# Performance work log

Hardware: AMD Instinct MI355X
Metric: run time of the kernel (lower is better)

## Reference

```python
import jax, jax.numpy as jnp
import numpy as np

NUM_HEADS = 16
HEAD_DIM = 64
TEMP = 0.001        # temperature for the mask-deriving softmax
THRESH = 0.019      # sparsity threshold
NEG = -1.0e9        # masked_fill value


def setup_inputs() -> dict:
    key = jax.random.key(0)
    ks = jax.random.split(key, 7)
    B, S, D = 4, 1024, 1024
    scale = 1.0 / np.sqrt(D).astype(np.float32)
    inp = {
        "Q": jax.random.normal(ks[0], (B, S, D), jnp.float32),
        "K": jax.random.normal(ks[1], (B, S, D), jnp.float32),
        "V": jax.random.normal(ks[2], (B, S, D), jnp.float32),
        "Wq": jax.random.normal(ks[3], (D, D), jnp.float32) * scale,
        "bq": jnp.zeros((D,), jnp.float32),
        "Wk": jax.random.normal(ks[4], (D, D), jnp.float32) * scale,
        "bk": jnp.zeros((D,), jnp.float32),
        "Wv": jax.random.normal(ks[5], (D, D), jnp.float32) * scale,
        "bv": jnp.zeros((D,), jnp.float32),
        "Wo": jax.random.normal(ks[6], (D, D), jnp.float32) * scale,
        "bo": jnp.zeros((D,), jnp.float32),
    }
    return inp


def reference(Q, K, V, Wq, bq, Wk, bk, Wv, bv, Wo, bo):
    B, S, D = Q.shape

    def split_heads(x):  # [B,S,D] -> [B,H,S,hd]
        return x.reshape(B, S, NUM_HEADS, HEAD_DIM).transpose(0, 2, 1, 3)

    q = split_heads(Q @ Wq + bq)
    k = split_heads(K @ Wk + bk)
    v = split_heads(V @ Wv + bv)

    scores = jnp.einsum('bhqd,bhkd->bhqk', q, k) / np.float32(np.sqrt(HEAD_DIM))
    # temperature-scaled softmax used only to derive a data-dependent mask
    att_map = jax.nn.softmax(scores / TEMP, axis=-1)
    masked_scores = jnp.where(att_map < THRESH, jnp.float32(NEG), scores)
    attn_weights = jax.nn.softmax(masked_scores, axis=-1)

    attn_out = jnp.einsum('bhqk,bhkd->bhqd', attn_weights, v)
    attn_out = attn_out.transpose(0, 2, 1, 3).reshape(B, S, D)
    return attn_out @ Wo + bo
```

## Files before the change

kernel.cpp:

```cpp
#include <hip/hip_runtime.h>
#include <hip/hip_bf16.h>
#include <math.h>

#define SEQ    1024
#define DMODEL 1024
#define NHEAD  16
#define HDIM   64
#define BATCH  4
#define MROWS  4096

typedef float f32x4 __attribute__((ext_vector_type(4)));
typedef short s16x8 __attribute__((ext_vector_type(8)));
typedef _Float16 f16x8 __attribute__((ext_vector_type(8)));

__device__ __forceinline__ float bf2f(unsigned short u) {
    return __uint_as_float(((unsigned int)u) << 16);
}
__device__ __forceinline__ unsigned short f2bf(float f) {
    __hip_bfloat16 h = __float2bfloat16(f);
    return *reinterpret_cast<unsigned short*>(&h);
}
__device__ __forceinline__ unsigned short f2h(float f) {
    _Float16 h = (_Float16)f;
    return *reinterpret_cast<unsigned short*>(&h);
}
__device__ __forceinline__ float h2f(unsigned short u) {
    _Float16 h = *reinterpret_cast<_Float16*>(&u);
    return (float)h;
}
__device__ __forceinline__ void split2(float x, unsigned short& u0, unsigned short& u1) {
    u0 = f2h(x);
    float f0 = h2f(u0);
    u1 = f2h((x - f0) * 2048.0f);
}

__device__ __forceinline__ void gload16(const void* g, void* l) {
    __builtin_amdgcn_global_load_lds(
        (const __attribute__((address_space(1))) unsigned int*)g,
        (__attribute__((address_space(3))) unsigned int*)l, 16, 0, 0);
}

template<int NS>
__global__ __launch_bounds__(256) void splitx_k(const float* __restrict__ X,
                                                unsigned short* __restrict__ P,
                                                int nvec, size_t plane)
{
    const int i = blockIdx.x * 256 + threadIdx.x;
    if (i >= nvec) return;
    const float* src = X + (size_t)i * 8;
    float4 v0 = *(const float4*)src;
    float4 v1 = *(const float4*)(src + 4);
    float x[8] = {v0.x, v0.y, v0.z, v0.w, v1.x, v1.y, v1.z, v1.w};
    unsigned short p0[8], p1[8];
    #pragma unroll
    for (int e = 0; e < 8; ++e) {
        if (NS == 1) { p0[e] = f2bf(x[e]); }
        else         { split2(x[e], p0[e], p1[e]); }
    }
    *(uint4*)(P + (size_t)i * 8) = *(uint4*)p0;
    if (NS == 2) {
        *(uint4*)(P + plane + (size_t)i * 8) = *(uint4*)p1;
    }
}

template<int NS>
__global__ __launch_bounds__(256) void wsplit_k(const float* __restrict__ W,
                                                unsigned short* __restrict__ Wt,
                                                size_t plane)
{
    __shared__ float tile[64][65];
    const int t  = threadIdx.x;
    const int n0 = blockIdx.x * 64;
    const int k0 = blockIdx.y * 64;
    const int col = t & 63;
    const int rq  = t >> 6;

    #pragma unroll
    for (int p = 0; p < 16; ++p) {
        const int row = p * 4 + rq;
        tile[row][col] = W[(size_t)(k0 + row) * DMODEL + n0 + col];
    }
    __syncthreads();
    #pragma unroll
    for (int p = 0; p < 16; ++p) {
        const int nrow = p * 4 + rq;
        const float v = tile[col][nrow];
        const size_t o = (size_t)(n0 + nrow) * DMODEL + k0 + col;
        if (NS == 1) {
            Wt[o] = f2bf(v);
        } else {
            unsigned short u0, u1;
            split2(v, u0, u1);
            Wt[o] = u0; Wt[plane + o] = u1;
        }
    }
}

template<int NS, bool FOLD, bool SPLITOUT>
__global__ __launch_bounds__(256, (NS == 1 ? 4 : 2))
void gemm_planes(const unsigned short* __restrict__ Ab,
                 const unsigned short* __restrict__ Bb,
                 const float* __restrict__ biasp,
                 float* __restrict__ Cp,
                 unsigned short* __restrict__ Pout,
                 float oscale,
                 int M, int N, int K,
                 size_t planeA, size_t planeB,
                 size_t planeO)
{
    __shared__ unsigned short S[2][NS][192][32];

    const int t = threadIdx.x;
    const int w = t >> 6, l = t & 63, g = l >> 4, j = l & 15;
    const int wm = w >> 1;
    const int wn = w & 1;
    const int m0 = blockIdx.y * 128;
    const int n0 = blockIdx.x * 64;

    f32x4 facc[8];
    #pragma unroll
    for (int f = 0; f < 8; ++f) facc[f] = (f32x4){0.f, 0.f, 0.f, 0.f};
    double dacc[8][4] = {};

    const int stgrow = w * 16 + (l >> 2);
    const int stgcol = ((l & 3) ^ ((l >> 3) & 3)) * 8;
    const unsigned short* gA = Ab + (size_t)(m0 + stgrow) * K + stgcol;
    const unsigned short* gB = Bb + (size_t)(n0 + stgrow) * K + stgcol;

    auto stage = [&](int buf, int k0) {
        #pragma unroll
        for (int p = 0; p < NS; ++p) {
            gload16(gA + (size_t)p * planeA + k0,                  &S[buf][p][w * 16][0]);
            gload16(gA + (size_t)p * planeA + (size_t)64 * K + k0, &S[buf][p][64 + w * 16][0]);
            gload16(gB + (size_t)p * planeB + k0,                  &S[buf][p][128 + w * 16][0]);
        }
    };

    const int gs8 = (g ^ ((j >> 1) & 3)) * 8;

    stage(0, 0);
    const int NT = K / 32;
    for (int kt = 0; kt < NT; ++kt) {
        const int cur = kt & 1;
        if (kt + 1 < NT) {
            stage(cur ^ 1, (kt + 1) * 32);
            if constexpr (NS == 2) asm volatile("s_waitcnt vmcnt(6)" ::: "memory");
            else                   asm volatile("s_waitcnt vmcnt(3)" ::: "memory");
        } else {
            asm volatile("s_waitcnt vmcnt(0)" ::: "memory");
        }
        __builtin_amdgcn_sched_barrier(0);
        __builtin_amdgcn_s_barrier();
        __builtin_amdgcn_sched_barrier(0);

        if constexpr (NS == 1) {
            s16x8 a[4];
            #pragma unroll
            for (int mi = 0; mi < 4; ++mi)
                a[mi] = *(const s16x8*)&S[cur][0][wm * 64 + mi * 16 + j][gs8];
            __builtin_amdgcn_s_setprio(1);
            #pragma unroll
            for (int ni = 0; ni < 2; ++ni) {
                const int nr = 128 + wn * 32 + ni * 16 + j;
                s16x8 b0 = *(const s16x8*)&S[cur][0][nr][gs8];
                #pragma unroll
                for (int mi = 0; mi < 4; ++mi) {
                    const int f = mi * 2 + ni;
                    facc[f] = __builtin_amdgcn_mfma_f32_16x16x32_bf16(a[mi], b0, facc[f], 0, 0, 0);
                }
            }
            __builtin_amdgcn_s_setprio(0);
        } else {
            f16x8 a0[4], a1[4];
            #pragma unroll
            for (int mi = 0; mi < 4; ++mi) {
                a0[mi] = *(const f16x8*)&S[cur][0][wm * 64 + mi * 16 + j][gs8];
                a1[mi] = *(const f16x8*)&S[cur][1][wm * 64 + mi * 16 + j][gs8];
            }
            __builtin_amdgcn_s_setprio(1);
            #pragma unroll
            for (int ni = 0; ni < 2; ++ni) {
                const int nr = 128 + wn * 32 + ni * 16 + j;
                f16x8 b0 = *(const f16x8*)&S[cur][0][nr][gs8];
                f16x8 b1 = *(const f16x8*)&S[cur][1][nr][gs8];
                #pragma unroll
                for (int mi = 0; mi < 4; ++mi) {
                    const int f = mi * 2 + ni;
                    f32x4 z = {0.f, 0.f, 0.f, 0.f};
                    z       = __builtin_amdgcn_mfma_f32_16x16x32_f16(a0[mi], b0, z,       0, 0, 0);
                    facc[f] = __builtin_amdgcn_mfma_f32_16x16x32_f16(a0[mi], b1, facc[f], 0, 0, 0);
                    facc[f] = __builtin_amdgcn_mfma_f32_16x16x32_f16(a1[mi], b0, facc[f], 0, 0, 0);
                    #pragma unroll
                    for (int r = 0; r < 4; ++r) dacc[f][r] += (double)z[r];
                }
            }
            __builtin_amdgcn_s_setprio(0);
        }

        __builtin_amdgcn_sched_barrier(0);
        __builtin_amdgcn_s_barrier();
        __builtin_amdgcn_sched_barrier(0);
    }

    #pragma unroll
    for (int ni = 0; ni < 2; ++ni) {
        const int col = n0 + wn * 32 + ni * 16 + j;
        const float bv = biasp[col];
        #pragma unroll
        for (int mi = 0; mi < 4; ++mi) {
            const int f = mi * 2 + ni;
            #pragma unroll
            for (int r = 0; r < 4; ++r) {
                const int row = m0 + wm * 64 + mi * 16 + 4 * g + r;
                float val;
                if (FOLD) val = (float)(dacc[f][r] + (double)facc[f][r] * (1.0 / 2048.0) + (double)bv);
                else      val = facc[f][r] + bv;
                if (SPLITOUT) {
                    const int bq = row >> 10, s = row & 1023;
                    const int h  = col >> 6,  d = col & 63;
                    const size_t o = (((size_t)(bq * 16 + h)) * SEQ + s) * HDIM + d;
                    unsigned short u0, u1;
                    split2(val * oscale, u0, u1);
                    Pout[o] = u0; Pout[planeO + o] = u1;
                } else {
                    Cp[(size_t)row * N + col] = val;
                }
            }
        }
    }
}

#define CAND 32
#define QROWS 128
__global__ __launch_bounds__(512, 4) void attn_k(const unsigned short* __restrict__ q3,
                                                 const unsigned short* __restrict__ k3,
                                                 const float* __restrict__ vf,
                                                 unsigned short* __restrict__ attnb,
                                                 size_t plane)
{
    __shared__ unsigned short Ks[2][64][72];
    __shared__ int   ckey[QROWS][CAND];
    __shared__ float csc[QROWS][CAND];
    __shared__ int   ccnt[QROWS];
    __shared__ float zinv[QROWS];

    const int t  = threadIdx.x;
    const int w  = t >> 6, l = t & 63, g = l >> 4, j = l & 15;
    const int bh = blockIdx.x >> 3;
    const int qt = blockIdx.x & 7;
    const int b  = bh >> 4, h = bh & 15;

    if (t < QROWS) ccnt[t] = 0;

    f16x8 aq[2][2];
    {
        const size_t qoff = ((size_t)bh * SEQ + qt * QROWS + w * 16 + j) * HDIM + g * 8;
        #pragma unroll
        for (int p = 0; p < 2; ++p)
            #pragma unroll
            for (int half = 0; half < 2; ++half)
                aq[p][half] = *(const f16x8*)(q3 + p * plane + qoff + half * 32);
    }

    const int skey = t >> 3;
    const int soff = (t & 7) * 8;
    const unsigned short* ksrc = k3 + (size_t)bh * (SEQ * HDIM) + (size_t)skey * HDIM + soff;

    float rm[4], rz[4];
    #pragma unroll
    for (int r = 0; r < 4; ++r) { rm[r] = -INFINITY; rz[r] = 0.f; }

    for (int ch = 0; ch < 16; ++ch) {
        __syncthreads();
        #pragma unroll
        for (int p = 0; p < 2; ++p) {
            const unsigned short* s = ksrc + p * plane + ch * 4096;
            *(uint4*)&Ks[p][skey][soff] = *(const uint4*)(s);
        }
        __syncthreads();

        float sc[4][4];
        __builtin_amdgcn_s_setprio(1);
        #pragma unroll
        for (int kb = 0; kb < 4; ++kb) {
            f32x4 accM = {0.f,0.f,0.f,0.f};
            f32x4 accC0 = {0.f,0.f,0.f,0.f}, accC1 = {0.f,0.f,0.f,0.f};
            const int kr = kb * 16 + j;
            #pragma unroll
            for (int half = 0; half < 2; ++half) {
                f16x8 b0 = *(const f16x8*)&Ks[0][kr][half * 32 + g * 8];
                f16x8 b1 = *(const f16x8*)&Ks[1][kr][half * 32 + g * 8];
                accM  = __builtin_amdgcn_mfma_f32_16x16x32_f16(aq[0][half], b0, accM,  0, 0, 0);
                accC0 = __builtin_amdgcn_mfma_f32_16x16x32_f16(aq[0][half], b1, accC0, 0, 0, 0);
                accC1 = __builtin_amdgcn_mfma_f32_16x16x32_f16(aq[1][half], b0, accC1, 0, 0, 0);
            }
            #pragma unroll
            for (int r = 0; r < 4; ++r)
                sc[kb][r] = accM[r] + (accC0[r] + accC1[r]) * (1.0f / 2048.0f);
        }
        __builtin_amdgcn_s_setprio(0);

        #pragma unroll
        for (int r = 0; r < 4; ++r) {
            float nmc = fmaxf(fmaxf(sc[0][r], sc[1][r]), fmaxf(sc[2][r], sc[3][r]));
            #pragma unroll
            for (int off = 1; off < 16; off <<= 1) nmc = fmaxf(nmc, __shfl_xor(nmc, off));
            if (__all(nmc <= rm[r] - 0.03f)) continue;
            const float nm = fmaxf(nmc, rm[r]);
            float add = 0.f;
            #pragma unroll
            for (int kb = 0; kb < 4; ++kb) add += __expf((sc[kb][r] - nm) * 1000.f);
            rz[r] = rz[r] * __expf((rm[r] - nm) * 1000.f) + add;
            rm[r] = nm;
            const float thr = nm - 0.004f;
            #pragma unroll
            for (int kb = 0; kb < 4; ++kb) {
                if (sc[kb][r] >= thr) {
                    const int row = w * 16 + 4 * g + r;
                    const int pos = atomicAdd(&ccnt[row], 1);
                    if (pos < CAND) {
                        ckey[row][pos] = ch * 64 + kb * 16 + j;
                        csc[row][pos]  = sc[kb][r];
                    }
                }
            }
        }
    }
    __syncthreads();

    float Zr[4];
    #pragma unroll
    for (int r = 0; r < 4; ++r) {
        float z = rz[r];
        #pragma unroll
        for (int off = 1; off < 16; off <<= 1) z += __shfl_xor(z, off);
        Zr[r] = z;
    }
    #pragma unroll
    for (int r = 0; r < 4; ++r) {
        if (j == r) {
            const int row = w * 16 + 4 * g + r;
            const double cut = (double)rm[r] + 0.001 * log(0.019 * (double)Zr[r]);
            const int craw = ccnt[row];
            const int c = craw < CAND ? craw : CAND;
            int n = 0; float z2 = 0.f;
            for (int i = 0; i < c; ++i) {
                const float s = csc[row][i];
                if ((double)s >= cut) {
                    const float ev = __expf(s - rm[r]);
                    ckey[row][n] = ckey[row][i];
                    csc[row][n]  = ev;
                    z2 += ev; ++n;
                }
            }
            ccnt[row] = (craw > CAND) ? -1 : n;
            zinv[row] = (n > 0) ? 1.f / z2 : 0.f;
        }
    }
    __syncthreads();

    const float* vbase = vf + (size_t)b * SEQ * DMODEL + h * HDIM + l;
    for (int i = 0; i < 16; ++i) {
        const int row = w * 16 + i;
        const int n = ccnt[row];
        float o = 0.f;
        if (n == 0) {
            for (int kk = 0; kk < SEQ; ++kk) o += vbase[(size_t)kk * DMODEL];
            o *= (1.0f / 1024.0f);
        } else if (n < 0) {
            o = INFINITY;
        } else {
            const float inv = zinv[row];
            int i2 = 0;
            for (; i2 + 4 <= n; i2 += 4) {
                const float c0 = csc[row][i2 + 0], c1 = csc[row][i2 + 1];
                const float c2 = csc[row][i2 + 2], c3 = csc[row][i2 + 3];
                const float v0 = vbase[(size_t)ckey[row][i2 + 0] * DMODEL];
                const float v1 = vbase[(size_t)ckey[row][i2 + 1] * DMODEL];
                const float v2 = vbase[(size_t)ckey[row][i2 + 2] * DMODEL];
                const float v3 = vbase[(size_t)ckey[row][i2 + 3] * DMODEL];
                o += c0 * v0; o += c1 * v1; o += c2 * v2; o += c3 * v3;
            }
            for (; i2 < n; ++i2)
                o += csc[row][i2] * vbase[(size_t)ckey[row][i2] * DMODEL];
            o *= inv;
        }
        attnb[((size_t)b * SEQ + qt * QROWS + row) * DMODEL + h * HDIM + l] = f2bf(o);
    }
}

extern "C" void kernel_launch(void* const* d_in, const int* in_sizes, int n_in,
                              void* d_out, int out_size, void* d_ws, size_t ws_size,
                              hipStream_t stream) {
    const float* Q  = (const float*)d_in[0];
    const float* K  = (const float*)d_in[1];
    const float* V  = (const float*)d_in[2];
    const float* Wq = (const float*)d_in[3];
    const float* bq = (const float*)d_in[4];
    const float* Wk = (const float*)d_in[5];
    const float* bk = (const float*)d_in[6];
    const float* Wv = (const float*)d_in[7];
    const float* bv = (const float*)d_in[8];
    const float* Wo = (const float*)d_in[9];
    const float* bo = (const float*)d_in[10];

    const size_t PLANE  = (size_t)MROWS * DMODEL;
    const size_t WPLANE = (size_t)DMODEL * DMODEL;

    unsigned short* Aspl = (unsigned short*)d_ws;
    unsigned short* Wp   = Aspl + 2 * PLANE;
    unsigned short* q3   = Wp + 2 * WPLANE;
    unsigned short* k3   = q3 + 2 * PLANE;
    float*          vf   = (float*)(k3 + 2 * PLANE);
    unsigned short* attnb = Aspl;

    dim3 blk(256, 1, 1);
    dim3 gg(DMODEL / 64, MROWS / 128, 1);
    dim3 gw(DMODEL / 64, DMODEL / 64, 1);
    const int nvec = (int)(PLANE / 8);
    dim3 gs((nvec + 255) / 256, 1, 1);

    splitx_k<2><<<gs, blk, 0, stream>>>(Q, Aspl, nvec, PLANE);
    wsplit_k<2><<<gw, blk, 0, stream>>>(Wq, Wp, WPLANE);
    gemm_planes<2, true, true><<<gg, blk, 0, stream>>>(Aspl, Wp, bq, nullptr, q3, 0.125f,
                                                       MROWS, DMODEL, DMODEL, PLANE, WPLANE, PLANE);
    splitx_k<2><<<gs, blk, 0, stream>>>(K, Aspl, nvec, PLANE);
    wsplit_k<2><<<gw, blk, 0, stream>>>(Wk, Wp, WPLANE);
    gemm_planes<2, true, true><<<gg, blk, 0, stream>>>(Aspl, Wp, bk, nullptr, k3, 1.0f,
                                                       MROWS, DMODEL, DMODEL, PLANE, WPLANE, PLANE);
    splitx_k<1><<<gs, blk, 0, stream>>>(V, Aspl, nvec, PLANE);
    wsplit_k<1><<<gw, blk, 0, stream>>>(Wv, Wp, WPLANE);
    gemm_planes<1, false, false><<<gg, blk, 0, stream>>>(Aspl, Wp, bv, vf, nullptr, 1.0f,
                                                         MROWS, DMODEL, DMODEL, PLANE, WPLANE, PLANE);
    attn_k<<<dim3(64 * 8, 1, 1), dim3(512, 1, 1), 0, stream>>>(q3, k3, vf, attnb, PLANE);

    wsplit_k<1><<<gw, blk, 0, stream>>>(Wo, Wp, WPLANE);
    gemm_planes<1, false, false><<<gg, blk, 0, stream>>>(attnb, Wp, bo, (float*)d_out, nullptr, 1.0f,
                                                         MROWS, DMODEL, DMODEL, PLANE, WPLANE, PLANE);
}
```

Measured before the change: 316.0 us.

## Batch Q and K projections into dual launches and prefetch K chunks in attention

The Q and K split, weight-transpose and GEMM kernels are merged into single launches that use a grid z/y dimension to pick the operand set. This doubles the grid so the GPU is better filled and cuts launch count. The workspace is re-laid out so separate buffers exist for each operand. The GEMM occupancy hint for the two-plane path rises from 2 to 3 waves per SIMD, and the attention kernel now register-prefetches the next K chunk while computing the current one. The costs are more workspace memory, possible register pressure from the higher occupancy bound, and dropped __restrict__ qualifiers on the GEMM inputs.

```diff
diff --git a/kernel.cpp b/kernel.cpp
--- a/kernel.cpp
+++ b/kernel.cpp
@@ -40,11 +40,16 @@
         (__attribute__((address_space(3))) unsigned int*)l, 16, 0, 0);
 }
 
-template<int NS>
-__global__ __launch_bounds__(256) void splitx_k(const float* __restrict__ X,
-                                                unsigned short* __restrict__ P,
+template<int NS, bool DUAL>
+__global__ __launch_bounds__(256) void splitx_k(const float* __restrict__ X0,
+                                                unsigned short* __restrict__ P0,
+                                                const float* __restrict__ X1,
+                                                unsigned short* __restrict__ P1,
                                                 int nvec, size_t plane)
 {
+    const float* X = X0;
+    unsigned short* P = P0;
+    if constexpr (DUAL) { if (blockIdx.y) { X = X1; P = P1; } }
     const int i = blockIdx.x * 256 + threadIdx.x;
     if (i >= nvec) return;
     const float* src = X + (size_t)i * 8;
@@ -63,11 +68,16 @@
     }
 }
 
-template<int NS>
-__global__ __launch_bounds__(256) void wsplit_k(const float* __restrict__ W,
-                                                unsigned short* __restrict__ Wt,
+template<int NS, bool DUAL>
+__global__ __launch_bounds__(256) void wsplit_k(const float* __restrict__ W0,
+                                                unsigned short* __restrict__ Wt0,
+                                                const float* __restrict__ W1,
+                                                unsigned short* __restrict__ Wt1,
                                                 size_t plane)
 {
+    const float* W = W0;
+    unsigned short* Wt = Wt0;
+    if constexpr (DUAL) { if (blockIdx.z) { W = W1; Wt = Wt1; } }
     __shared__ float tile[64][65];
     const int t  = threadIdx.x;
     const int n0 = blockIdx.x * 64;
@@ -96,18 +106,25 @@
     }
 }
 
-template<int NS, bool FOLD, bool SPLITOUT>
-__global__ __launch_bounds__(256, (NS == 1 ? 4 : 2))
-void gemm_planes(const unsigned short* __restrict__ Ab,
-                 const unsigned short* __restrict__ Bb,
-                 const float* __restrict__ biasp,
-                 float* __restrict__ Cp,
-                 unsigned short* __restrict__ Pout,
-                 float oscale,
+template<int NS, bool FOLD, bool SPLITOUT, bool DUAL>
+__global__ __launch_bounds__(256, (NS == 1 ? 4 : 3))
+void gemm_planes(const unsigned short* Ab0, const unsigned short* Bb0,
+                 const float* bias0, float* __restrict__ Cp,
+                 unsigned short* Pout0, float oscale0,
+                 const unsigned short* Ab1, const unsigned short* Bb1,
+                 const float* bias1, unsigned short* Pout1, float oscale1,
                  int M, int N, int K,
-                 size_t planeA, size_t planeB,
-                 size_t planeO)
+                 size_t planeA, size_t planeB, size_t planeO)
 {
+    const unsigned short* Ab = Ab0;
+    const unsigned short* Bb = Bb0;
+    const float* biasp = bias0;
+    unsigned short* Pout = Pout0;
+    float oscale = oscale0;
+    if constexpr (DUAL) {
+        if (blockIdx.z) { Ab = Ab1; Bb = Bb1; biasp = bias1; Pout = Pout1; oscale = oscale1; }
+    }
+
     __shared__ unsigned short S[2][NS][192][32];
 
     const int t = threadIdx.x;
@@ -270,14 +287,19 @@
     #pragma unroll
     for (int r = 0; r < 4; ++r) { rm[r] = -INFINITY; rz[r] = 0.f; }
 
+    uint4 stg0 = *(const uint4*)(ksrc);
+    uint4 stg1 = *(const uint4*)(ksrc + plane);
+
     for (int ch = 0; ch < 16; ++ch) {
         __syncthreads();
-        #pragma unroll
-        for (int p = 0; p < 2; ++p) {
-            const unsigned short* s = ksrc + p * plane + ch * 4096;
-            *(uint4*)&Ks[p][skey][soff] = *(const uint4*)(s);
-        }
+        *(uint4*)&Ks[0][skey][soff] = stg0;
+        *(uint4*)&Ks[1][skey][soff] = stg1;
         __syncthreads();
+        if (ch + 1 < 16) {
+            const unsigned short* s = ksrc + (ch + 1) * 4096;
+            stg0 = *(const uint4*)(s);
+            stg1 = *(const uint4*)(s + plane);
+        }
 
         float sc[4][4];
         __builtin_amdgcn_s_setprio(1);
@@ -407,34 +429,44 @@
     const size_t PLANE  = (size_t)MROWS * DMODEL;
     const size_t WPLANE = (size_t)DMODEL * DMODEL;
 
-    unsigned short* Aspl = (unsigned short*)d_ws;
-    unsigned short* Wp   = Aspl + 2 * PLANE;
-    unsigned short* q3   = Wp + 2 * WPLANE;
-    unsigned short* k3   = q3 + 2 * PLANE;
-    float*          vf   = (float*)(k3 + 2 * PLANE);
-    unsigned short* attnb = Aspl;
+    unsigned short* R1 = (unsigned short*)d_ws;
+    unsigned short* R2 = R1 + 2 * PLANE;
+    unsigned short* W1 = R2 + 2 * PLANE;
+    unsigned short* W2 = W1 + WPLANE;
+    unsigned short* W3 = W2 + 2 * WPLANE;
+    unsigned short* q3 = W3 + 2 * WPLANE;
+    unsigned short* k3 = q3 + 2 * PLANE;
+    float*          vf = (float*)(k3 + 2 * PLANE);
+    unsigned short* attnb = R1;
 
     dim3 blk(256, 1, 1);
-    dim3 gg(DMODEL / 64, MROWS / 128, 1);
-    dim3 gw(DMODEL / 64, DMODEL / 64, 1);
     const int nvec = (int)(PLANE / 8);
     dim3 gs((nvec + 255) / 256, 1, 1);
-
-    splitx_k<2><<<gs, blk, 0, stream>>>(Q, Aspl, nvec, PLANE);
-    wsplit_k<2><<<gw, blk, 0, stream>>>(Wq, Wp, WPLANE);
-    gemm_planes<2, true, true><<<gg, blk, 0, stream>>>(Aspl, Wp, bq, nullptr, q3, 0.125f,
-                                                       MROWS, DMODEL, DMODEL, PLANE, WPLANE, PLANE);
-    splitx_k<2><<<gs, blk, 0, stream>>>(K, Aspl, nvec, PLANE);
-    wsplit_k<2><<<gw, blk, 0, stream>>>(Wk, Wp, WPLANE);
-    gemm_planes<2, true, true><<<gg, blk, 0, stream>>>(Aspl, Wp, bk, nullptr, k3, 1.0f,
-                                                       MROWS, DMODEL, DMODEL, PLANE, WPLANE, PLANE);
-    splitx_k<1><<<gs, blk, 0, stream>>>(V, Aspl, nvec, PLANE);
-    wsplit_k<1><<<gw, blk, 0, stream>>>(Wv, Wp, WPLANE);
-    gemm_planes<1, false, false><<<gg, blk, 0, stream>>>(Aspl, Wp, bv, vf, nullptr, 1.0f,
-                                                         MROWS, DMODEL, DMODEL, PLANE, WPLANE, PLANE);
+    dim3 gs2((nvec + 255) / 256, 2, 1);
+    dim3 gw(DMODEL / 64, DMODEL / 64, 1);
+    dim3 gw2(DMODEL / 64, DMODEL / 64, 2);
+    dim3 gg(DMODEL / 64, MROWS / 128, 1);
+    dim3 gg2(DMODEL / 64, MROWS / 128, 2);
+
+    splitx_k<1, false><<<gs, blk, 0, stream>>>(V, R1, nullptr, nullptr, nvec, PLANE);
+    wsplit_k<1, false><<<gw, blk, 0, stream>>>(Wv, W1, nullptr, nullptr, WPLANE);
+    gemm_planes<1, false, false, false><<<gg, blk, 0, stream>>>(
+        R1, W1, bv, vf, nullptr, 1.0f,
+        nullptr, nullptr, nullptr, nullptr, 0.f,
+        MROWS, DMODEL, DMODEL, PLANE, WPLANE, PLANE);
+
+    splitx_k<2, true><<<gs2, blk, 0, stream>>>(Q, R1, K, R2, nvec, PLANE);
+    wsplit_k<2, true><<<gw2, blk, 0, stream>>>(Wq, W2, Wk, W3, WPLANE);
+    gemm_planes<2, true, true, true><<<gg2, blk, 0, stream>>>(
+        R1, W2, bq, nullptr, q3, 0.125f,
+        R2, W3, bk, k3, 1.0f,
+        MROWS, DMODEL, DMODEL, PLANE, WPLANE, PLANE);
+
     attn_k<<<dim3(64 * 8, 1, 1), dim3(512, 1, 1), 0, stream>>>(q3, k3, vf, attnb, PLANE);
 
-    wsplit_k<1><<<gw, blk, 0, stream>>>(Wo, Wp, WPLANE);
-    gemm_planes<1, false, false><<<gg, blk, 0, stream>>>(attnb, Wp, bo, (float*)d_out, nullptr, 1.0f,
-                                                         MROWS, DMODEL, DMODEL, PLANE, WPLANE, PLANE);
-}
+    wsplit_k<1, false><<<gw, blk, 0, stream>>>(Wo, W1, nullptr, nullptr, WPLANE);
+    gemm_planes<1, false, false, false><<<gg, blk, 0, stream>>>(
+        attnb, W1, bo, (float*)d_out, nullptr, 1.0f,
+        nullptr, nullptr, nullptr, nullptr, 0.f,
+        MROWS, DMODEL, DMODEL, PLANE, WPLANE, PLANE);
+}
```

After: 299.4 us. 5.2% less time.
